# Performance work log

Hardware: AMD Instinct MI355X
Metric: run time of the kernel (lower is better)

The kernel has to match this reference:

```python
import jax, jax.numpy as jnp
import numpy as np
import math

IN_DIM = 1024
L = 4096
D_MODEL = 512
D_INNER = 1024   # expand=2 * d_model
D_STATE = 16
D_CONV = 4
DT_RANK = 32     # ceil(d_model / 16)
N_LAYERS = 2
RATE = 10


def setup_inputs() -> dict:
    key = jax.random.key(0)
    ks = iter(jax.random.split(key, 32))
    def w(shape, fan_in):
        return jax.random.normal(next(ks), shape, jnp.float32) * (1.0 / math.sqrt(fan_in))
    return {
        "x": jax.random.normal(next(ks), (1, L, IN_DIM), jnp.float32),
        "rate": RATE,
        "fc1_w": w((D_MODEL, IN_DIM), IN_DIM),
        "fc1_b": jnp.zeros((D_MODEL,), jnp.float32),
        "ln_w": jnp.ones((N_LAYERS, D_MODEL), jnp.float32),
        "ln_b": jnp.zeros((N_LAYERS, D_MODEL), jnp.float32),
        "in_proj_w": w((N_LAYERS, 2 * D_INNER, D_MODEL), D_MODEL),
        "conv_w": w((N_LAYERS, D_INNER, D_CONV), D_CONV),
        "conv_b": jnp.zeros((N_LAYERS, D_INNER), jnp.float32),
        "x_proj_w": w((N_LAYERS, DT_RANK + 2 * D_STATE, D_INNER), D_INNER),
        "dt_proj_w": w((N_LAYERS, D_INNER, DT_RANK), DT_RANK),
        "dt_proj_b": jax.random.normal(next(ks), (N_LAYERS, D_INNER), jnp.float32) * 0.1,
        "A_log": jnp.tile(jnp.log(jnp.arange(1, D_STATE + 1, dtype=jnp.float32)), (N_LAYERS, D_INNER, 1)),
        "D_skip": jnp.ones((N_LAYERS, D_INNER), jnp.float32),
        "out_proj_w": w((N_LAYERS, D_MODEL, D_INNER), D_INNER),
        "norm_w": jnp.ones((D_MODEL,), jnp.float32),
        "norm_b": jnp.zeros((D_MODEL,), jnp.float32),
        "attn_w1": w((128, D_MODEL), D_MODEL),
        "attn_b1": jnp.zeros((128,), jnp.float32),
        "attn_w2": w((1, 128), 128),
        "attn_b2": jnp.zeros((1,), jnp.float32),
        "out2048_w": w((2048, D_MODEL), D_MODEL),
        "out2048_b": jnp.zeros((2048,), jnp.float32),
    }


def _layernorm(x, w, b, eps=1e-5):
    mu = x.mean(-1, keepdims=True)
    var = ((x - mu) ** 2).mean(-1, keepdims=True)
    return (x - mu) * jax.lax.rsqrt(var + eps) * w + b


def _causal_conv(x, w, b):
    # depthwise causal conv: x [L, d], w [d, K] -> y[t, d] = sum_k w[d, k] * x[t - (K-1) + k, d]
    K = w.shape[1]
    xp = jnp.pad(x, ((K - 1, 0), (0, 0)))
    y = sum(xp[k:k + x.shape[0]] * w[:, k] for k in range(K))
    return y + b


def _selective_scan(u, dt, A, B, C, Dp, z):
    # u, dt, z: [L, d]; A: [d, n]; B, C: [L, n]; Dp: [d]
    def step(h, inp):
        dt_t, B_t, C_t, u_t = inp
        dA = jnp.exp(dt_t[:, None] * A)                    # [d, n]
        h = dA * h + (dt_t * u_t)[:, None] * B_t[None, :]  # [d, n]
        return h, h @ C_t                                  # y_t: [d]
    h0 = jnp.zeros((u.shape[1], A.shape[1]), u.dtype)
    _, y = jax.lax.scan(step, h0, (dt, B, C, u))
    return (y + u * Dp) * jax.nn.silu(z)


def _srmamba(h, perm, inv, in_w, cw, cb, xw, dtw, dtb, A_log, Dp, ow):
    xz = h @ in_w.T                         # [L, 2*d_inner]
    x, z = jnp.split(xz, 2, axis=-1)
    x, z = x[perm], z[perm]                 # sequence reordering (stride `rate`)
    x = jax.nn.silu(_causal_conv(x, cw, cb))
    dbl = x @ xw.T                          # [L, dt_rank + 2n]
    dt = jax.nn.softplus(dbl[:, :DT_RANK] @ dtw.T + dtb)
    B = dbl[:, DT_RANK:DT_RANK + D_STATE]
    C = dbl[:, DT_RANK + D_STATE:]
    y = _selective_scan(x, dt, -jnp.exp(A_log), B, C, Dp, z)
    return y[inv] @ ow.T                    # restore original order, out_proj


def reference(x, rate, fc1_w, fc1_b, ln_w, ln_b, in_proj_w, conv_w, conv_b, x_proj_w, dt_proj_w, dt_proj_b, A_log, D_skip, out_proj_w, norm_w, norm_b, attn_w1, attn_b1, attn_w2, attn_b2, out2048_w, out2048_b):
    h = jax.nn.relu(x[0] @ fc1_w.T + fc1_b)   # [L, 512]
    Lx = h.shape[0]
    perm = jnp.concatenate([jnp.arange(i, Lx, rate) for i in range(rate)])
    inv = jnp.argsort(perm)
    for l in range(N_LAYERS):
        h = h + _srmamba(_layernorm(h, ln_w[l], ln_b[l]), perm, inv,
                         in_proj_w[l], conv_w[l], conv_b[l], x_proj_w[l],
                         dt_proj_w[l], dt_proj_b[l], A_log[l], D_skip[l], out_proj_w[l])
    h = _layernorm(h, norm_w, norm_b)
    a = jnp.tanh(h @ attn_w1.T + attn_b1) @ attn_w2.T + attn_b2  # [L, 1]
    Aatt = jax.nn.softmax(a[:, 0])                                # [L]
    pooled = Aatt @ h                                             # [512]
    out = pooled @ out2048_w.T + out2048_b                        # [2048]
    return out[None, :], Aatt[None, None, :]
```

## Files before the change

### kernel.cpp

```cpp
#include <hip/hip_runtime.h>
#include <hip/hip_fp16.h>
#include <math.h>

#define L 4096
#define DIN 1024
#define DM 512
#define DI 1024
#define DS 16
#define DTR 32
#define NCH 128
#define CHK 32

typedef _Float16 v8h __attribute__((ext_vector_type(8)));
typedef float v4f __attribute__((ext_vector_type(4)));

__global__ void perm_k(int* __restrict__ perm, const int* __restrict__ ratep) {
    int p = blockIdx.x * blockDim.x + threadIdx.x;
    if (p >= L) return;
    int rate = ratep[0];
    int cum = 0;
    for (int g = 0; g < rate; ++g) {
        int sz = (L - g + rate - 1) / rate;
        if (p < cum + sz) { perm[p] = g + rate * (p - cum); return; }
        cum += sz;
    }
}

__global__ __launch_bounds__(256) void f2h_k(
    const float* __restrict__ in, _Float16* __restrict__ out)
{
    int i = (blockIdx.x * 256 + threadIdx.x) * 4;
    float4 v = *(const float4*)(in + i);
    _Float16 h4[4] = {(_Float16)v.x, (_Float16)v.y, (_Float16)v.z, (_Float16)v.w};
    *(uint2*)(out + i) = *(uint2*)h4;
}

__global__ __launch_bounds__(256) void zero4_k(float* __restrict__ p) {
    int i = (blockIdx.x * 256 + threadIdx.x) * 4;
    *(float4*)(p + i) = make_float4(0.f, 0.f, 0.f, 0.f);
}

template<int ACT, int BNT>
__global__ __launch_bounds__(256) void hgemm_nt(
    const _Float16* __restrict__ A, int lda,
    const _Float16* __restrict__ B, int ldb,
    float* __restrict__ C, int ldc,
    const float* __restrict__ bias, int K, int accum)
{
    constexpr int MI = (BNT == 128) ? 4 : 2;
    __shared__ _Float16 As[128][40];
    __shared__ _Float16 Bs[BNT][40];
    int tid = threadIdx.x;
    int m0 = blockIdx.y * 128, n0 = blockIdx.x * BNT;
    int lane = tid & 63, wave = tid >> 6;
    int wm, wn;
    if constexpr (BNT == 128) { wm = (wave >> 1) * 64; wn = (wave & 1) * 64; }
    else                      { wm = wave * 32;        wn = 0; }
    int quad = lane >> 4, r16 = lane & 15;
    v4f acc[MI][4] = {};

    int srow = tid >> 1;
    int scol = (tid & 1) * 16;
    const _Float16* Ag = A + (size_t)(m0 + srow) * lda + scol;
    int srowB = (BNT == 128) ? srow : (tid >> 2);
    int scolB = (BNT == 128) ? scol : (tid & 3) * 8;
    const _Float16* Bg = B + (size_t)(n0 + srowB) * ldb + scolB;

    uint4 a0, a1, b0, b1;
    a0 = *(const uint4*)(Ag);
    a1 = *(const uint4*)(Ag + 8);
    b0 = *(const uint4*)(Bg);
    if constexpr (BNT == 128) b1 = *(const uint4*)(Bg + 8);

    int KS = K / 32;
    for (int ks = 0; ks < KS; ++ks) {
        __syncthreads();
        *(uint4*)&As[srow][scol] = a0;
        *(uint4*)&As[srow][scol + 8] = a1;
        *(uint4*)&Bs[srowB][scolB] = b0;
        if constexpr (BNT == 128) *(uint4*)&Bs[srowB][scolB + 8] = b1;
        __syncthreads();
        if (ks + 1 < KS) {
            int k0 = (ks + 1) * 32;
            a0 = *(const uint4*)(Ag + k0);
            a1 = *(const uint4*)(Ag + k0 + 8);
            b0 = *(const uint4*)(Bg + k0);
            if constexpr (BNT == 128) b1 = *(const uint4*)(Bg + k0 + 8);
        }
        v8h af[MI], bf[4];
#pragma unroll
        for (int i = 0; i < MI; ++i)
            af[i] = *(const v8h*)&As[wm + i * 16 + r16][quad * 8];
#pragma unroll
        for (int j = 0; j < 4; ++j)
            bf[j] = *(const v8h*)&Bs[wn + j * 16 + r16][quad * 8];
#pragma unroll
        for (int i = 0; i < MI; ++i)
#pragma unroll
            for (int j = 0; j < 4; ++j)
                acc[i][j] = __builtin_amdgcn_mfma_f32_16x16x32_f16(
                    af[i], bf[j], acc[i][j], 0, 0, 0);
    }

#pragma unroll
    for (int i = 0; i < MI; ++i) {
#pragma unroll
        for (int j = 0; j < 4; ++j) {
            int col = n0 + wn + j * 16 + r16;
            int rbase = m0 + wm + i * 16 + quad * 4;
            float bv = bias ? bias[col] : 0.f;
#pragma unroll
            for (int r = 0; r < 4; ++r) {
                float v = acc[i][j][r] + bv;
                if (ACT == 1) v = fmaxf(v, 0.f);
                float* p = C + (size_t)(rbase + r) * ldc + col;
                if (accum) v += *p;
                *p = v;
            }
        }
    }
}

#define BM 64
#define BN 64
#define BKK 32
template<int ACT>
__global__ __launch_bounds__(256) void gemm_nt(
    const float* __restrict__ A, int lda,
    const float* __restrict__ B, int ldb,
    float* __restrict__ C, int ldc,
    const float* __restrict__ bias,
    int M, int N, int K, int kchunk, int accum)
{
    __shared__ float As[BKK][BM + 4];
    __shared__ float Bs[BKK][BN + 4];
    int tid = threadIdx.x;
    int m0 = blockIdx.y * BM;
    int n0 = blockIdx.x * BN;
    int tx = tid & 15, ty = tid >> 4;
    float acc[4][4] = {};
    int arow = tid >> 3;
    int ak = (tid & 7) * 4;
    int kb = blockIdx.z * kchunk;
    int ke = min(K, kb + kchunk);

    for (int k0 = kb; k0 < ke; k0 += BKK) {
#pragma unroll
        for (int r = 0; r < 2; ++r) {
            int row = arow + r * 32;
            float4 va = *(const float4*)(A + (size_t)(m0 + row) * lda + k0 + ak);
            As[ak + 0][row] = va.x; As[ak + 1][row] = va.y;
            As[ak + 2][row] = va.z; As[ak + 3][row] = va.w;
            float4 vb = *(const float4*)(B + (size_t)(n0 + row) * ldb + k0 + ak);
            Bs[ak + 0][row] = vb.x; Bs[ak + 1][row] = vb.y;
            Bs[ak + 2][row] = vb.z; Bs[ak + 3][row] = vb.w;
        }
        __syncthreads();
#pragma unroll
        for (int kk = 0; kk < BKK; ++kk) {
            float4 a4 = *(const float4*)&As[kk][ty * 4];
            float4 b4 = *(const float4*)&Bs[kk][tx * 4];
            float a[4] = {a4.x, a4.y, a4.z, a4.w};
            float b[4] = {b4.x, b4.y, b4.z, b4.w};
#pragma unroll
            for (int i = 0; i < 4; ++i)
#pragma unroll
                for (int j = 0; j < 4; ++j)
                    acc[i][j] = fmaf(a[i], b[j], acc[i][j]);
        }
        __syncthreads();
    }

#pragma unroll
    for (int i = 0; i < 4; ++i) {
        int row = m0 + ty * 4 + i;
        int col = n0 + tx * 4;
        float* cp = C + (size_t)row * ldc + col;
        if (accum == 2) {
#pragma unroll
            for (int j = 0; j < 4; ++j) atomicAdd(cp + j, acc[i][j]);
            continue;
        }
        float v[4];
#pragma unroll
        for (int j = 0; j < 4; ++j) {
            float x = acc[i][j] + (bias ? bias[col + j] : 0.f);
            if (ACT == 2) x = (x > 20.f) ? x : log1pf(expf(x));
            else if (ACT == 3) x = tanhf(x);
            v[j] = x;
        }
        if (accum == 1) {
#pragma unroll
            for (int j = 0; j < 4; ++j) v[j] += cp[j];
        }
#pragma unroll
        for (int j = 0; j < 4; ++j) cp[j] = v[j];
    }
}

__global__ __launch_bounds__(256) void layernorm_k(
    const float* __restrict__ x, const float* __restrict__ w,
    const float* __restrict__ b, float* __restrict__ o,
    _Float16* __restrict__ oh)
{
    int row = blockIdx.x;
    int tid = threadIdx.x;
    const float* xr = x + (size_t)row * DM;
    float v0 = xr[tid], v1 = xr[tid + 256];
    float s = v0 + v1, ss = v0 * v0 + v1 * v1;
    for (int off = 32; off; off >>= 1) {
        s += __shfl_down(s, off, 64);
        ss += __shfl_down(ss, off, 64);
    }
    __shared__ float sm[4], sm2[4];
    int wave = tid >> 6, lane = tid & 63;
    if (lane == 0) { sm[wave] = s; sm2[wave] = ss; }
    __syncthreads();
    float tot = sm[0] + sm[1] + sm[2] + sm[3];
    float tot2 = sm2[0] + sm2[1] + sm2[2] + sm2[3];
    float mu = tot * (1.f / DM);
    float var = tot2 * (1.f / DM) - mu * mu;
    float rs = rsqrtf(var + 1e-5f);
    float y0 = (v0 - mu) * rs * w[tid] + b[tid];
    float y1 = (v1 - mu) * rs * w[tid + 256] + b[tid + 256];
    o[(size_t)row * DM + tid] = y0;
    o[(size_t)row * DM + tid + 256] = y1;
    if (oh) {
        oh[(size_t)row * DM + tid] = (_Float16)y0;
        oh[(size_t)row * DM + tid + 256] = (_Float16)y1;
    }
}

__global__ __launch_bounds__(256) void conv_silu_k(
    const float* __restrict__ xz, const int* __restrict__ perm,
    const float* __restrict__ cw, const float* __restrict__ cb,
    float* __restrict__ xc)
{
    int g = blockIdx.x * 256 + threadIdx.x;
    int c = g & (DI - 1), p = g >> 10;
    float acc = cb[c];
#pragma unroll
    for (int k = 0; k < 4; ++k) {
        int q = p + k - 3;
        if (q >= 0)
            acc = fmaf(xz[(size_t)perm[q] * (2 * DI) + c], cw[c * 4 + k], acc);
    }
    float sig = 1.f / (1.f + __expf(-acc));
    xc[g] = acc * sig;
}

__global__ __launch_bounds__(256) void scan_pass1(
    const float* __restrict__ dt, const float* __restrict__ u,
    const float* __restrict__ dbl, const float* __restrict__ A_log,
    float* __restrict__ Aprod, float* __restrict__ carry)
{
    int c = blockIdx.x * 256 + threadIdx.x;
    int j = blockIdx.y;
    float Ac[16];
#pragma unroll
    for (int s = 0; s < 16; ++s) Ac[s] = -__expf(A_log[c * DS + s]);
    float ap[16], h[16];
#pragma unroll
    for (int s = 0; s < 16; ++s) { ap[s] = 1.f; h[s] = 0.f; }
    int t0 = j * CHK;
    for (int tt = 0; tt < CHK; ++tt) {
        int t = t0 + tt;
        float dtv = dt[(size_t)t * DI + c];
        float uv  = u[(size_t)t * DI + c];
        v4f Bv[4];
#pragma unroll
        for (int q = 0; q < 4; ++q)
            Bv[q] = *(const v4f*)(dbl + (size_t)t * 64 + DTR + q * 4);
        float du = dtv * uv;
#pragma unroll
        for (int s = 0; s < 16; ++s) {
            float dA = __expf(dtv * Ac[s]);
            h[s] = fmaf(dA, h[s], du * Bv[s >> 2][s & 3]);
            ap[s] *= dA;
        }
    }
    size_t base = ((size_t)j * DI + c) * DS;
#pragma unroll
    for (int q = 0; q < 4; ++q) {
        *(v4f*)(Aprod + base + q * 4) = *(v4f*)&ap[q * 4];
        *(v4f*)(carry + base + q * 4) = *(v4f*)&h[q * 4];
    }
}

__global__ __launch_bounds__(256) void scan_pass2(
    const float* __restrict__ Aprod, const float* __restrict__ carry,
    float* __restrict__ Hin)
{
    int idx = blockIdx.x * 256 + threadIdx.x;
    float H = 0.f;
    Hin[idx] = 0.f;
    for (int j = 1; j < NCH; ++j) {
        H = fmaf(Aprod[(size_t)(j - 1) * (DI * DS) + idx], H,
                 carry[(size_t)(j - 1) * (DI * DS) + idx]);
        Hin[(size_t)j * (DI * DS) + idx] = H;
    }
}

__global__ __launch_bounds__(256) void scan_pass3(
    const float* __restrict__ dt, const float* __restrict__ u,
    const float* __restrict__ dbl, const float* __restrict__ xz,
    const float* __restrict__ A_log, const float* __restrict__ Dsk,
    const int* __restrict__ perm, const float* __restrict__ Hin,
    _Float16* __restrict__ yo)
{
    int c = blockIdx.x * 256 + threadIdx.x;
    int j = blockIdx.y;
    float Ac[16];
#pragma unroll
    for (int s = 0; s < 16; ++s) Ac[s] = -__expf(A_log[c * DS + s]);
    float Dp = Dsk[c];
    float h[16];
    size_t hbase = ((size_t)j * DI + c) * DS;
#pragma unroll
    for (int q = 0; q < 4; ++q)
        *(v4f*)&h[q * 4] = *(const v4f*)(Hin + hbase + q * 4);
    int t0 = j * CHK;
    for (int tt = 0; tt < CHK; ++tt) {
        int t = t0 + tt;
        float dtv = dt[(size_t)t * DI + c];
        float uv  = u[(size_t)t * DI + c];
        v4f Bv[4], Cv[4];
#pragma unroll
        for (int q = 0; q < 4; ++q) {
            Bv[q] = *(const v4f*)(dbl + (size_t)t * 64 + DTR + q * 4);
            Cv[q] = *(const v4f*)(dbl + (size_t)t * 64 + DTR + DS + q * 4);
        }
        float du = dtv * uv;
        float y = 0.f;
#pragma unroll
        for (int s = 0; s < 16; ++s) {
            float dA = __expf(dtv * Ac[s]);
            h[s] = fmaf(dA, h[s], du * Bv[s >> 2][s & 3]);
            y = fmaf(h[s], Cv[s >> 2][s & 3], y);
        }
        int tp = perm[t];
        float z = xz[(size_t)tp * (2 * DI) + DI + c];
        float sig = 1.f / (1.f + __expf(-z));
        yo[(size_t)tp * DI + c] = (_Float16)((y + uv * Dp) * (z * sig));
    }
}

__global__ __launch_bounds__(256) void attnscore_k(
    const float* __restrict__ t1, const float* __restrict__ w2,
    const float* __restrict__ b2, float* __restrict__ avec)
{
    int t = blockIdx.x * 256 + threadIdx.x;
    const float* r = t1 + (size_t)t * 128;
    float acc = 0.f;
#pragma unroll 8
    for (int j = 0; j < 128; ++j) acc = fmaf(r[j], w2[j], acc);
    avec[t] = acc + b2[0];
}

__global__ __launch_bounds__(1024) void softmax_k(
    const float* __restrict__ a, float* __restrict__ out)
{
    int tid = threadIdx.x;
    float v[4];
    float mx = -1e30f;
#pragma unroll
    for (int i = 0; i < 4; ++i) { v[i] = a[tid + i * 1024]; mx = fmaxf(mx, v[i]); }
    __shared__ float sm[16];
    for (int off = 32; off; off >>= 1) mx = fmaxf(mx, __shfl_xor(mx, off, 64));
    int wave = tid >> 6, lane = tid & 63;
    if (lane == 0) sm[wave] = mx;
    __syncthreads();
    if (tid < 16) {
        float m = sm[tid];
        for (int off = 8; off; off >>= 1) m = fmaxf(m, __shfl_xor(m, off, 64));
        sm[tid] = m;
    }
    __syncthreads();
    mx = sm[0];
    float s = 0.f;
#pragma unroll
    for (int i = 0; i < 4; ++i) { v[i] = __expf(v[i] - mx); s += v[i]; }
    for (int off = 32; off; off >>= 1) s += __shfl_xor(s, off, 64);
    __syncthreads();
    if (lane == 0) sm[wave] = s;
    __syncthreads();
    if (tid < 16) {
        float t2 = sm[tid];
        for (int off = 8; off; off >>= 1) t2 += __shfl_xor(t2, off, 64);
        sm[tid] = t2;
    }
    __syncthreads();
    float inv = 1.f / sm[0];
#pragma unroll
    for (int i = 0; i < 4; ++i) out[tid + i * 1024] = v[i] * inv;
}

__global__ void zero_k(float* p, int n) {
    int i = blockIdx.x * 256 + threadIdx.x;
    if (i < n) p[i] = 0.f;
}

__global__ __launch_bounds__(512) void pool_k(
    const float* __restrict__ aatt, const float* __restrict__ h,
    float* __restrict__ pooled)
{
    int m = threadIdx.x;
    int t0 = blockIdx.x * 128;
    float acc = 0.f;
    for (int r = 0; r < 128; ++r) {
        int t = t0 + r;
        acc = fmaf(aatt[t], h[(size_t)t * DM + m], acc);
    }
    atomicAdd(&pooled[m], acc);
}

__global__ __launch_bounds__(64) void out2048_k(
    const float* __restrict__ pooled, const float* __restrict__ w,
    const float* __restrict__ b, float* __restrict__ out)
{
    int n = blockIdx.x;
    int lane = threadIdx.x;
    const float* wr = w + (size_t)n * DM;
    float acc = 0.f;
#pragma unroll
    for (int k = 0; k < 8; ++k)
        acc = fmaf(wr[lane + k * 64], pooled[lane + k * 64], acc);
    for (int off = 32; off; off >>= 1) acc += __shfl_xor(acc, off, 64);
    if (lane == 0) out[n] = acc + b[n];
}

extern "C" void kernel_launch(void* const* d_in, const int* in_sizes, int n_in,
                              void* d_out, int out_size, void* d_ws, size_t ws_size,
                              hipStream_t stream) {
    const float* x     = (const float*)d_in[0];
    const int*   rate  = (const int*)d_in[1];
    const float* fc1_w = (const float*)d_in[2];
    const float* fc1_b = (const float*)d_in[3];
    const float* ln_w  = (const float*)d_in[4];
    const float* ln_b  = (const float*)d_in[5];
    const float* ipw   = (const float*)d_in[6];
    const float* cw    = (const float*)d_in[7];
    const float* cb    = (const float*)d_in[8];
    const float* xpw   = (const float*)d_in[9];
    const float* dtw   = (const float*)d_in[10];
    const float* dtpb  = (const float*)d_in[11];
    const float* A_log = (const float*)d_in[12];
    const float* Dsk   = (const float*)d_in[13];
    const float* opw   = (const float*)d_in[14];
    const float* nw    = (const float*)d_in[15];
    const float* nb    = (const float*)d_in[16];
    const float* aw1   = (const float*)d_in[17];
    const float* ab1   = (const float*)d_in[18];
    const float* aw2   = (const float*)d_in[19];
    const float* ab2   = (const float*)d_in[20];
    const float* ow    = (const float*)d_in[21];
    const float* ob    = (const float*)d_in[22];
    float* out = (float*)d_out;

    int* perm = (int*)d_ws;
    float* f = (float*)d_ws + 4096;
    float* h    = f; f += (size_t)L * DM;
    float* hln  = f; f += (size_t)L * DM;
    float* xz   = f; f += (size_t)L * 2 * DI;
    float* xc   = f; f += (size_t)L * DI;
    float* dbl  = f; f += (size_t)L * 64;
    float* dtv  = f; f += (size_t)L * DI;
    float* t1   = f; f += (size_t)L * 128;
    float* avec = f; f += L;
    float* pooled = f; f += DM;
    float* Aprod = f; f += (size_t)NCH * DI * DS;
    float* carry = f; f += (size_t)NCH * DI * DS;
    float* Hin   = f; f += (size_t)NCH * DI * DS;
    _Float16* fh = (_Float16*)f;
    _Float16* xh     = fh; fh += (size_t)L * DIN;
    _Float16* hln_h  = fh; fh += (size_t)L * DM;
    _Float16* yo_h   = fh; fh += (size_t)L * DI;
    _Float16* fc1w_h = fh; fh += (size_t)DM * DIN;
    _Float16* ipw_h  = fh; fh += (size_t)2 * 2 * DI * DM;
    _Float16* opw_h  = fh; fh += (size_t)2 * DM * DI;

    perm_k<<<16, 256, 0, stream>>>(perm, rate);

    f2h_k<<<L * DIN / 1024, 256, 0, stream>>>(x, xh);
    f2h_k<<<DM * DIN / 1024, 256, 0, stream>>>(fc1_w, fc1w_h);
    f2h_k<<<2 * 2 * DI * DM / 1024, 256, 0, stream>>>(ipw, ipw_h);
    f2h_k<<<2 * DM * DI / 1024, 256, 0, stream>>>(opw, opw_h);

    hgemm_nt<1, 64><<<dim3(DM / 64, L / 128), 256, 0, stream>>>(
        xh, DIN, fc1w_h, DIN, h, DM, fc1_b, DIN, 0);

    for (int l = 0; l < 2; ++l) {
        layernorm_k<<<L, 256, 0, stream>>>(h, ln_w + l * DM, ln_b + l * DM, hln, hln_h);
        hgemm_nt<0, 128><<<dim3(2 * DI / 128, L / 128), 256, 0, stream>>>(
            hln_h, DM, ipw_h + (size_t)l * 2 * DI * DM, DM, xz, 2 * DI,
            nullptr, DM, 0);
        conv_silu_k<<<L * DI / 256, 256, 0, stream>>>(
            xz, perm, cw + (size_t)l * DI * 4, cb + (size_t)l * DI, xc);
        zero4_k<<<L * 64 / 1024, 256, 0, stream>>>(dbl);
        gemm_nt<0><<<dim3(1, L / 64, 4), 256, 0, stream>>>(
            xc, DI, xpw + (size_t)l * 64 * DI, DI, dbl, 64, nullptr,
            L, 64, DI, DI / 4, 2);
        gemm_nt<2><<<dim3(DI / 64, L / 64), 256, 0, stream>>>(
            dbl, 64, dtw + (size_t)l * DI * DTR, DTR, dtv, DI,
            dtpb + (size_t)l * DI, L, DI, DTR, DTR, 0);
        scan_pass1<<<dim3(DI / 256, NCH), 256, 0, stream>>>(
            dtv, xc, dbl, A_log + (size_t)l * DI * DS, Aprod, carry);
        scan_pass2<<<DI * DS / 256, 256, 0, stream>>>(Aprod, carry, Hin);
        scan_pass3<<<dim3(DI / 256, NCH), 256, 0, stream>>>(
            dtv, xc, dbl, xz, A_log + (size_t)l * DI * DS, Dsk + (size_t)l * DI,
            perm, Hin, yo_h);
        hgemm_nt<0, 64><<<dim3(DM / 64, L / 128), 256, 0, stream>>>(
            yo_h, DI, opw_h + (size_t)l * DM * DI, DI, h, DM, nullptr, DI, 1);
    }

    layernorm_k<<<L, 256, 0, stream>>>(h, nw, nb, hln, nullptr);
    gemm_nt<3><<<dim3(128 / 64, L / 64), 256, 0, stream>>>(
        hln, DM, aw1, DM, t1, 128, ab1, L, 128, DM, DM, 0);
    attnscore_k<<<L / 256, 256, 0, stream>>>(t1, aw2, ab2, avec);
    softmax_k<<<1, 1024, 0, stream>>>(avec, out + 2048);
    zero_k<<<2, 256, 0, stream>>>(pooled, DM);
    pool_k<<<32, 512, 0, stream>>>(out + 2048, hln, pooled);
    out2048_k<<<2048, 64, 0, stream>>>(pooled, ow, ob, out);
}
```

Measured before the change: 608.8 us.

## Fuse dt projection into scans, store xz in fp16, merge small kernels

Removes the separate dt_proj GEMM; each scan pass now recomputes dt per timestep from the dbl row and the dt_proj weights held in registers. The in_proj output xz is written in fp16 to halve its traffic, and the four fp16 conversions are merged into one launch. Zeroing of dbl, avec and pooled is folded into existing kernels, and the attention tanh plus score dot is fused into the GEMM epilogue using atomics. This cuts launches and the large dt round trip, at the cost of extra ALU work and registers in the scans and lower precision on xz.

```diff
diff --git a/kernel.cpp b/kernel.cpp
--- a/kernel.cpp
+++ b/kernel.cpp
@@ -26,25 +26,29 @@
     }
 }
 
-__global__ __launch_bounds__(256) void f2h_k(
-    const float* __restrict__ in, _Float16* __restrict__ out)
-{
-    int i = (blockIdx.x * 256 + threadIdx.x) * 4;
-    float4 v = *(const float4*)(in + i);
+__global__ __launch_bounds__(256) void f2h_multi_k(
+    const float* __restrict__ s0, _Float16* __restrict__ d0, int b0,
+    const float* __restrict__ s1, _Float16* __restrict__ d1, int b1,
+    const float* __restrict__ s2, _Float16* __restrict__ d2, int b2,
+    const float* __restrict__ s3, _Float16* __restrict__ d3, int b3)
+{
+    int b = blockIdx.x;
+    const float* src; _Float16* dst; int lb;
+    if (b < b0)                { src = s0; dst = d0; lb = b; }
+    else if (b < b0 + b1)      { src = s1; dst = d1; lb = b - b0; }
+    else if (b < b0 + b1 + b2) { src = s2; dst = d2; lb = b - b0 - b1; }
+    else                       { src = s3; dst = d3; lb = b - b0 - b1 - b2; }
+    int i = (lb * 256 + threadIdx.x) * 4;
+    float4 v = *(const float4*)(src + i);
     _Float16 h4[4] = {(_Float16)v.x, (_Float16)v.y, (_Float16)v.z, (_Float16)v.w};
-    *(uint2*)(out + i) = *(uint2*)h4;
-}
-
-__global__ __launch_bounds__(256) void zero4_k(float* __restrict__ p) {
-    int i = (blockIdx.x * 256 + threadIdx.x) * 4;
-    *(float4*)(p + i) = make_float4(0.f, 0.f, 0.f, 0.f);
-}
-
-template<int ACT, int BNT>
+    *(uint2*)(dst + i) = *(uint2*)h4;
+}
+
+template<int ACT, int BNT, int HALF>
 __global__ __launch_bounds__(256) void hgemm_nt(
     const _Float16* __restrict__ A, int lda,
     const _Float16* __restrict__ B, int ldb,
-    float* __restrict__ C, int ldc,
+    void* __restrict__ Cv, int ldc,
     const float* __restrict__ bias, int K, int accum)
 {
     constexpr int MI = (BNT == 128) ? 4 : 2;
@@ -113,9 +117,13 @@
             for (int r = 0; r < 4; ++r) {
                 float v = acc[i][j][r] + bv;
                 if (ACT == 1) v = fmaxf(v, 0.f);
-                float* p = C + (size_t)(rbase + r) * ldc + col;
-                if (accum) v += *p;
-                *p = v;
+                if constexpr (HALF) {
+                    ((_Float16*)Cv)[(size_t)(rbase + r) * ldc + col] = (_Float16)v;
+                } else {
+                    float* p = (float*)Cv + (size_t)(rbase + r) * ldc + col;
+                    if (accum) v += *p;
+                    *p = v;
+                }
             }
         }
     }
@@ -130,7 +138,8 @@
     const float* __restrict__ B, int ldb,
     float* __restrict__ C, int ldc,
     const float* __restrict__ bias,
-    int M, int N, int K, int kchunk, int accum)
+    int M, int N, int K, int kchunk, int accum,
+    const float* __restrict__ w2, float* __restrict__ avec)
 {
     __shared__ float As[BKK][BM + 4];
     __shared__ float Bs[BKK][BN + 4];
@@ -175,33 +184,33 @@
     for (int i = 0; i < 4; ++i) {
         int row = m0 + ty * 4 + i;
         int col = n0 + tx * 4;
+        if (ACT == 4) {
+            float part = 0.f;
+#pragma unroll
+            for (int j = 0; j < 4; ++j) {
+                float xv = tanhf(acc[i][j] + bias[col + j]);
+                part = fmaf(xv, w2[col + j], part);
+            }
+            atomicAdd(&avec[row], part);
+            continue;
+        }
         float* cp = C + (size_t)row * ldc + col;
         if (accum == 2) {
 #pragma unroll
             for (int j = 0; j < 4; ++j) atomicAdd(cp + j, acc[i][j]);
             continue;
         }
-        float v[4];
-#pragma unroll
-        for (int j = 0; j < 4; ++j) {
-            float x = acc[i][j] + (bias ? bias[col + j] : 0.f);
-            if (ACT == 2) x = (x > 20.f) ? x : log1pf(expf(x));
-            else if (ACT == 3) x = tanhf(x);
-            v[j] = x;
-        }
-        if (accum == 1) {
-#pragma unroll
-            for (int j = 0; j < 4; ++j) v[j] += cp[j];
-        }
-#pragma unroll
-        for (int j = 0; j < 4; ++j) cp[j] = v[j];
+#pragma unroll
+        for (int j = 0; j < 4; ++j)
+            cp[j] = acc[i][j] + (bias ? bias[col + j] : 0.f);
     }
 }
 
 __global__ __launch_bounds__(256) void layernorm_k(
     const float* __restrict__ x, const float* __restrict__ w,
     const float* __restrict__ b, float* __restrict__ o,
-    _Float16* __restrict__ oh)
+    _Float16* __restrict__ oh, float* __restrict__ avec,
+    const float* __restrict__ b2)
 {
     int row = blockIdx.x;
     int tid = threadIdx.x;
@@ -229,13 +238,18 @@
         oh[(size_t)row * DM + tid] = (_Float16)y0;
         oh[(size_t)row * DM + tid + 256] = (_Float16)y1;
     }
+    if (avec && tid == 0) avec[row] = b2[0];
 }
 
 __global__ __launch_bounds__(256) void conv_silu_k(
-    const float* __restrict__ xz, const int* __restrict__ perm,
+    const _Float16* __restrict__ xz, const int* __restrict__ perm,
     const float* __restrict__ cw, const float* __restrict__ cb,
-    float* __restrict__ xc)
-{
+    float* __restrict__ xc, float* __restrict__ dbl)
+{
+    if (blockIdx.x < 256) {
+        int zi = (blockIdx.x * 256 + threadIdx.x) * 4;
+        *(float4*)(dbl + zi) = make_float4(0.f, 0.f, 0.f, 0.f);
+    }
     int g = blockIdx.x * 256 + threadIdx.x;
     int c = g & (DI - 1), p = g >> 10;
     float acc = cb[c];
@@ -243,15 +257,29 @@
     for (int k = 0; k < 4; ++k) {
         int q = p + k - 3;
         if (q >= 0)
-            acc = fmaf(xz[(size_t)perm[q] * (2 * DI) + c], cw[c * 4 + k], acc);
+            acc = fmaf((float)xz[(size_t)perm[q] * (2 * DI) + c], cw[c * 4 + k], acc);
     }
     float sig = 1.f / (1.f + __expf(-acc));
     xc[g] = acc * sig;
 }
 
+__device__ __forceinline__ float dt_of(
+    const float* __restrict__ dblrow, const v4f* __restrict__ dw, float dtbc)
+{
+    float dot = dtbc;
+#pragma unroll
+    for (int q = 0; q < 8; ++q) {
+        v4f dr = *(const v4f*)(dblrow + q * 4);
+#pragma unroll
+        for (int r = 0; r < 4; ++r) dot = fmaf(dr[r], dw[q][r], dot);
+    }
+    return (dot > 20.f) ? dot : log1pf(__expf(dot));
+}
+
 __global__ __launch_bounds__(256) void scan_pass1(
-    const float* __restrict__ dt, const float* __restrict__ u,
-    const float* __restrict__ dbl, const float* __restrict__ A_log,
+    const float* __restrict__ u, const float* __restrict__ dbl,
+    const float* __restrict__ dtw, const float* __restrict__ dtb,
+    const float* __restrict__ A_log,
     float* __restrict__ Aprod, float* __restrict__ carry)
 {
     int c = blockIdx.x * 256 + threadIdx.x;
@@ -259,18 +287,23 @@
     float Ac[16];
 #pragma unroll
     for (int s = 0; s < 16; ++s) Ac[s] = -__expf(A_log[c * DS + s]);
+    v4f dw[8];
+#pragma unroll
+    for (int q = 0; q < 8; ++q) dw[q] = *(const v4f*)(dtw + c * DTR + q * 4);
+    float dtbc = dtb[c];
     float ap[16], h[16];
 #pragma unroll
     for (int s = 0; s < 16; ++s) { ap[s] = 1.f; h[s] = 0.f; }
     int t0 = j * CHK;
     for (int tt = 0; tt < CHK; ++tt) {
         int t = t0 + tt;
-        float dtv = dt[(size_t)t * DI + c];
+        const float* dblrow = dbl + (size_t)t * 64;
+        float dtv = dt_of(dblrow, dw, dtbc);
         float uv  = u[(size_t)t * DI + c];
         v4f Bv[4];
 #pragma unroll
         for (int q = 0; q < 4; ++q)
-            Bv[q] = *(const v4f*)(dbl + (size_t)t * 64 + DTR + q * 4);
+            Bv[q] = *(const v4f*)(dblrow + DTR + q * 4);
         float du = dtv * uv;
 #pragma unroll
         for (int s = 0; s < 16; ++s) {
@@ -302,17 +335,21 @@
 }
 
 __global__ __launch_bounds__(256) void scan_pass3(
-    const float* __restrict__ dt, const float* __restrict__ u,
-    const float* __restrict__ dbl, const float* __restrict__ xz,
-    const float* __restrict__ A_log, const float* __restrict__ Dsk,
-    const int* __restrict__ perm, const float* __restrict__ Hin,
-    _Float16* __restrict__ yo)
+    const float* __restrict__ u, const float* __restrict__ dbl,
+    const float* __restrict__ dtw, const float* __restrict__ dtb,
+    const _Float16* __restrict__ xz, const float* __restrict__ A_log,
+    const float* __restrict__ Dsk, const int* __restrict__ perm,
+    const float* __restrict__ Hin, _Float16* __restrict__ yo)
 {
     int c = blockIdx.x * 256 + threadIdx.x;
     int j = blockIdx.y;
     float Ac[16];
 #pragma unroll
     for (int s = 0; s < 16; ++s) Ac[s] = -__expf(A_log[c * DS + s]);
+    v4f dw[8];
+#pragma unroll
+    for (int q = 0; q < 8; ++q) dw[q] = *(const v4f*)(dtw + c * DTR + q * 4);
+    float dtbc = dtb[c];
     float Dp = Dsk[c];
     float h[16];
     size_t hbase = ((size_t)j * DI + c) * DS;
@@ -322,13 +359,14 @@
     int t0 = j * CHK;
     for (int tt = 0; tt < CHK; ++tt) {
         int t = t0 + tt;
-        float dtv = dt[(size_t)t * DI + c];
+        const float* dblrow = dbl + (size_t)t * 64;
+        float dtv = dt_of(dblrow, dw, dtbc);
         float uv  = u[(size_t)t * DI + c];
         v4f Bv[4], Cv[4];
 #pragma unroll
         for (int q = 0; q < 4; ++q) {
-            Bv[q] = *(const v4f*)(dbl + (size_t)t * 64 + DTR + q * 4);
-            Cv[q] = *(const v4f*)(dbl + (size_t)t * 64 + DTR + DS + q * 4);
+            Bv[q] = *(const v4f*)(dblrow + DTR + q * 4);
+            Cv[q] = *(const v4f*)(dblrow + DTR + DS + q * 4);
         }
         float du = dtv * uv;
         float y = 0.f;
@@ -339,28 +377,18 @@
             y = fmaf(h[s], Cv[s >> 2][s & 3], y);
         }
         int tp = perm[t];
-        float z = xz[(size_t)tp * (2 * DI) + DI + c];
+        float z = (float)xz[(size_t)tp * (2 * DI) + DI + c];
         float sig = 1.f / (1.f + __expf(-z));
         yo[(size_t)tp * DI + c] = (_Float16)((y + uv * Dp) * (z * sig));
     }
 }
 
-__global__ __launch_bounds__(256) void attnscore_k(
-    const float* __restrict__ t1, const float* __restrict__ w2,
-    const float* __restrict__ b2, float* __restrict__ avec)
-{
-    int t = blockIdx.x * 256 + threadIdx.x;
-    const float* r = t1 + (size_t)t * 128;
-    float acc = 0.f;
-#pragma unroll 8
-    for (int j = 0; j < 128; ++j) acc = fmaf(r[j], w2[j], acc);
-    avec[t] = acc + b2[0];
-}
-
 __global__ __launch_bounds__(1024) void softmax_k(
-    const float* __restrict__ a, float* __restrict__ out)
+    const float* __restrict__ a, float* __restrict__ out,
+    float* __restrict__ pooled)
 {
     int tid = threadIdx.x;
+    if (tid < DM) pooled[tid] = 0.f;
     float v[4];
     float mx = -1e30f;
 #pragma unroll
@@ -393,11 +421,6 @@
     float inv = 1.f / sm[0];
 #pragma unroll
     for (int i = 0; i < 4; ++i) out[tid + i * 1024] = v[i] * inv;
-}
-
-__global__ void zero_k(float* p, int n) {
-    int i = blockIdx.x * 256 + threadIdx.x;
-    if (i < n) p[i] = 0.f;
 }
 
 __global__ __launch_bounds__(512) void pool_k(
@@ -461,11 +484,8 @@
     float* f = (float*)d_ws + 4096;
     float* h    = f; f += (size_t)L * DM;
     float* hln  = f; f += (size_t)L * DM;
-    float* xz   = f; f += (size_t)L * 2 * DI;
     float* xc   = f; f += (size_t)L * DI;
     float* dbl  = f; f += (size_t)L * 64;
-    float* dtv  = f; f += (size_t)L * DI;
-    float* t1   = f; f += (size_t)L * 128;
     float* avec = f; f += L;
     float* pooled = f; f += DM;
     float* Aprod = f; f += (size_t)NCH * DI * DS;
@@ -475,50 +495,50 @@
     _Float16* xh     = fh; fh += (size_t)L * DIN;
     _Float16* hln_h  = fh; fh += (size_t)L * DM;
     _Float16* yo_h   = fh; fh += (size_t)L * DI;
+    _Float16* xz_h   = fh; fh += (size_t)L * 2 * DI;
     _Float16* fc1w_h = fh; fh += (size_t)DM * DIN;
     _Float16* ipw_h  = fh; fh += (size_t)2 * 2 * DI * DM;
     _Float16* opw_h  = fh; fh += (size_t)2 * DM * DI;
 
     perm_k<<<16, 256, 0, stream>>>(perm, rate);
 
-    f2h_k<<<L * DIN / 1024, 256, 0, stream>>>(x, xh);
-    f2h_k<<<DM * DIN / 1024, 256, 0, stream>>>(fc1_w, fc1w_h);
-    f2h_k<<<2 * 2 * DI * DM / 1024, 256, 0, stream>>>(ipw, ipw_h);
-    f2h_k<<<2 * DM * DI / 1024, 256, 0, stream>>>(opw, opw_h);
-
-    hgemm_nt<1, 64><<<dim3(DM / 64, L / 128), 256, 0, stream>>>(
+    f2h_multi_k<<<(L * DIN + DM * DIN + 2 * 2 * DI * DM + 2 * DM * DI) / 1024,
+                  256, 0, stream>>>(
+        x, xh, L * DIN / 1024,
+        fc1_w, fc1w_h, DM * DIN / 1024,
+        ipw, ipw_h, 2 * 2 * DI * DM / 1024,
+        opw, opw_h, 2 * DM * DI / 1024);
+
+    hgemm_nt<1, 64, 0><<<dim3(DM / 64, L / 128), 256, 0, stream>>>(
         xh, DIN, fc1w_h, DIN, h, DM, fc1_b, DIN, 0);
 
     for (int l = 0; l < 2; ++l) {
-        layernorm_k<<<L, 256, 0, stream>>>(h, ln_w + l * DM, ln_b + l * DM, hln, hln_h);
-        hgemm_nt<0, 128><<<dim3(2 * DI / 128, L / 128), 256, 0, stream>>>(
-            hln_h, DM, ipw_h + (size_t)l * 2 * DI * DM, DM, xz, 2 * DI,
+        layernorm_k<<<L, 256, 0, stream>>>(h, ln_w + l * DM, ln_b + l * DM,
+                                           hln, hln_h, nullptr, nullptr);
+        hgemm_nt<0, 128, 1><<<dim3(2 * DI / 128, L / 128), 256, 0, stream>>>(
+            hln_h, DM, ipw_h + (size_t)l * 2 * DI * DM, DM, xz_h, 2 * DI,
             nullptr, DM, 0);
         conv_silu_k<<<L * DI / 256, 256, 0, stream>>>(
-            xz, perm, cw + (size_t)l * DI * 4, cb + (size_t)l * DI, xc);
-        zero4_k<<<L * 64 / 1024, 256, 0, stream>>>(dbl);
+            xz_h, perm, cw + (size_t)l * DI * 4, cb + (size_t)l * DI, xc, dbl);
         gemm_nt<0><<<dim3(1, L / 64, 4), 256, 0, stream>>>(
             xc, DI, xpw + (size_t)l * 64 * DI, DI, dbl, 64, nullptr,
-            L, 64, DI, DI / 4, 2);
-        gemm_nt<2><<<dim3(DI / 64, L / 64), 256, 0, stream>>>(
-            dbl, 64, dtw + (size_t)l * DI * DTR, DTR, dtv, DI,
-            dtpb + (size_t)l * DI, L, DI, DTR, DTR, 0);
+            L, 64, DI, DI / 4, 2, nullptr, nullptr);
         scan_pass1<<<dim3(DI / 256, NCH), 256, 0, stream>>>(
-            dtv, xc, dbl, A_log + (size_t)l * DI * DS, Aprod, carry);
+            xc, dbl, dtw + (size_t)l * DI * DTR, dtpb + (size_t)l * DI,
+            A_log + (size_t)l * DI * DS, Aprod, carry);
         scan_pass2<<<DI * DS / 256, 256, 0, stream>>>(Aprod, carry, Hin);
         scan_pass3<<<dim3(DI / 256, NCH), 256, 0, stream>>>(
-            dtv, xc, dbl, xz, A_log + (size_t)l * DI * DS, Dsk + (size_t)l * DI,
+            xc, dbl, dtw + (size_t)l * DI * DTR, dtpb + (size_t)l * DI,
+            xz_h, A_log + (size_t)l * DI * DS, Dsk + (size_t)l * DI,
             perm, Hin, yo_h);
-        hgemm_nt<0, 64><<<dim3(DM / 64, L / 128), 256, 0, stream>>>(
+        hgemm_nt<0, 64, 0><<<dim3(DM / 64, L / 128), 256, 0, stream>>>(
             yo_h, DI, opw_h + (size_t)l * DM * DI, DI, h, DM, nullptr, DI, 1);
     }
 
-    layernorm_k<<<L, 256, 0, stream>>>(h, nw, nb, hln, nullptr);
-    gemm_nt<3><<<dim3(128 / 64, L / 64), 256, 0, stream>>>(
-        hln, DM, aw1, DM, t1, 128, ab1, L, 128, DM, DM, 0);
-    attnscore_k<<<L / 256, 256, 0, stream>>>(t1, aw2, ab2, avec);
-    softmax_k<<<1, 1024, 0, stream>>>(avec, out + 2048);
-    zero_k<<<2, 256, 0, stream>>>(pooled, DM);
+    layernorm_k<<<L, 256, 0, stream>>>(h, nw, nb, hln, nullptr, avec, ab2);
+    gemm_nt<4><<<dim3(128 / 64, L / 64), 256, 0, stream>>>(
+        hln, DM, aw1, DM, nullptr, 0, ab1, L, 128, DM, DM, 0, aw2, avec);
+    softmax_k<<<1, 1024, 0, stream>>>(avec, out + 2048, pooled);
     pool_k<<<32, 512, 0, stream>>>(out + 2048, hln, pooled);
     out2048_k<<<2048, 64, 0, stream>>>(pooled, ow, ob, out);
 }
```

Result: no change. 620.0 us (+1.8%).
